# Performance work log

Hardware: AMD Instinct MI355X
Metric: run time of the kernel (lower is better)

Reference implementation:

```python
import jax, jax.numpy as jnp
import numpy as np

N_NODES = 100000
N_EDGES = 1600000
D_IN, D_HID, D_OUT = 64, 128, 64


def setup_inputs() -> dict:
    key = jax.random.key(0)
    ks = jax.random.split(key, 12)
    s = lambda d: 1.0 / np.sqrt(d)
    return {
        "x": jax.random.normal(ks[0], (N_NODES, D_IN), dtype=jnp.float32),
        "edge_index": jax.random.randint(ks[1], (2, N_EDGES), 0, N_NODES, dtype=jnp.int64),
        # conv1 MLP: Linear(D_IN->D_HID), ReLU, Linear(D_HID->D_HID)
        "W1a": jax.random.uniform(ks[2], (D_IN, D_HID), jnp.float32, -s(D_IN), s(D_IN)),
        "b1a": jnp.zeros((D_HID,), jnp.float32),
        "W1b": jax.random.uniform(ks[3], (D_HID, D_HID), jnp.float32, -s(D_HID), s(D_HID)),
        "b1b": jnp.zeros((D_HID,), jnp.float32),
        # conv2 MLP: Linear(D_HID->D_HID), ReLU, Linear(D_HID->D_HID)
        "W2a": jax.random.uniform(ks[4], (D_HID, D_HID), jnp.float32, -s(D_HID), s(D_HID)),
        "b2a": jnp.zeros((D_HID,), jnp.float32),
        "W2b": jax.random.uniform(ks[5], (D_HID, D_HID), jnp.float32, -s(D_HID), s(D_HID)),
        "b2b": jnp.zeros((D_HID,), jnp.float32),
        # final projection Linear(D_HID->D_OUT)
        "Wlin": jax.random.uniform(ks[6], (D_HID, D_OUT), jnp.float32, -s(D_HID), s(D_HID)),
        "blin": jnp.zeros((D_OUT,), jnp.float32),
    }


def _gin_conv(h, src, dst, Wa, ba, Wb, bb, num_nodes):
    # GINConv (eps=0): MLP((1+eps)*x + sum_{j->i} x_j)
    agg = jax.ops.segment_sum(h[src], dst, num_segments=num_nodes)  # [N, d]
    z = h + agg
    z = jax.nn.relu(z @ Wa + ba)
    return z @ Wb + bb


def reference(x, edge_index, W1a, b1a, W1b, b1b, W2a, b2a, W2b, b2b, Wlin, blin):
    n = x.shape[0]
    src, dst = edge_index[0], edge_index[1]
    h = jax.nn.relu(_gin_conv(x, src, dst, W1a, b1a, W1b, b1b, n))
    h = jax.nn.relu(_gin_conv(h, src, dst, W2a, b2a, W2b, b2b, n))
    return h @ Wlin + blin  # [N, D_OUT]
```

## Files before the change

kernel.cpp:

```cpp
#include <hip/hip_runtime.h>
#include <hip/hip_fp16.h>


typedef __attribute__((ext_vector_type(8))) short short8;
typedef __attribute__((ext_vector_type(8))) _Float16 half8;
typedef __attribute__((ext_vector_type(4))) float f32x4;
union F8 { unsigned u[4]; uint4 u4; short8 s; half8 h; };


constexpr int BUCKET_SHIFT = 9;
constexpr int BUCKET_NODES = 1 << BUCKET_SHIFT;
constexpr int CAP = 10240;
constexpr int EPB = 2048;
constexpr int NBUCK_MAX = 256;

__global__ __launch_bounds__(256) void bucket_scatter_kernel(const int* __restrict__ ei, int E,
                                                             int* __restrict__ gcur,
                                                             int* __restrict__ gpk,
                                                             int nbuck) {
    __shared__ int spk[EPB];
    __shared__ unsigned char sbuck[EPB];
    __shared__ int lcnt[NBUCK_MAX];
    __shared__ int lbase[NBUCK_MAX];
    __shared__ int lcur[NBUCK_MAX];
    __shared__ int gbase[NBUCK_MAX];
    __shared__ int stmp[256];

    const int t = threadIdx.x;
    const int e0 = blockIdx.x * EPB;
    const int ecnt = min(EPB, E - e0);

    for (int i = t; i < NBUCK_MAX; i += 256) lcnt[i] = 0;
    __syncthreads();

    for (int i = t; i < ecnt; i += 256) {
        int d = ei[E + e0 + i];
        atomicAdd(&lcnt[d >> BUCKET_SHIFT], 1);
    }
    __syncthreads();

    int v = lcnt[t];
    stmp[t] = v;
    __syncthreads();
    #pragma unroll
    for (int off = 1; off < 256; off <<= 1) {
        int add = (t >= off) ? stmp[t - off] : 0;
        __syncthreads();
        stmp[t] += add;
        __syncthreads();
    }
    lbase[t] = stmp[t] - v;
    lcur[t] = stmp[t] - v;
    __syncthreads();

    for (int i = t; i < ecnt; i += 256) {
        int s = ei[e0 + i];
        int d = ei[E + e0 + i];
        int b = d >> BUCKET_SHIFT;
        int p = atomicAdd(&lcur[b], 1);
        spk[p] = ((d & (BUCKET_NODES - 1)) << 17) | s;
        sbuck[p] = (unsigned char)b;
    }
    __syncthreads();

    if (t < nbuck) {
        int c = lcnt[t];
        gbase[t] = (c > 0) ? atomicAdd(&gcur[t], c) : 0;
    }
    __syncthreads();

    for (int i = t; i < ecnt; i += 256) {
        int b = sbuck[i];
        int gp = gbase[b] + (i - lbase[b]);
        if (gp < (b + 1) * CAP) gpk[gp] = spk[i];
    }
}

__global__ __launch_bounds__(1024) void bucket_build_kernel(const int* __restrict__ gpk,
                                                            const int* __restrict__ gcur,
                                                            int* __restrict__ row_start,
                                                            int* __restrict__ edge_src,
                                                            int N, int E, int nbuck) {
    __shared__ int h[BUCKET_NODES];
    __shared__ int s[BUCKET_NODES];
    __shared__ int sb[NBUCK_MAX];
    __shared__ int bbase_sh;
    const int t = threadIdx.x;
    const int b = blockIdx.x;
    const int base = b << BUCKET_SHIFT;

    if (t < NBUCK_MAX) {
        int c = 0;
        if (t < nbuck) c = min(gcur[t] - t * CAP, CAP);
        sb[t] = c;
    }
    for (int i = t; i < BUCKET_NODES; i += 1024) h[i] = 0;
    __syncthreads();
    #pragma unroll
    for (int off = 1; off < NBUCK_MAX; off <<= 1) {
        int add = (t >= off && t < NBUCK_MAX) ? sb[t - off] : 0;
        __syncthreads();
        if (t < NBUCK_MAX) sb[t] += add;
        __syncthreads();
    }
    if (t == 0) {
        int cb0 = min(gcur[b] - b * CAP, CAP);
        bbase_sh = sb[b] - cb0;
    }

    int cb = min(gcur[b] - b * CAP, CAP);
    const int* pp = gpk + (size_t)b * CAP;
    for (int i = t; i < cb; i += 1024) atomicAdd(&h[((unsigned)pp[i]) >> 17], 1);
    __syncthreads();

    int c0 = (t < BUCKET_NODES) ? h[t] : 0;
    if (t < BUCKET_NODES) s[t] = c0;
    __syncthreads();
    #pragma unroll
    for (int off = 1; off < BUCKET_NODES; off <<= 1) {
        int add = (t >= off && t < BUCKET_NODES) ? s[t - off] : 0;
        __syncthreads();
        if (t < BUCKET_NODES) s[t] += add;
        __syncthreads();
    }
    if (t < BUCKET_NODES) {
        int ex = s[t] - c0 + bbase_sh;
        h[t] = ex;
        if (base + t < N) row_start[base + t] = ex;
    }
    if (b == 0 && t == 0) row_start[N] = E;
    __syncthreads();

    for (int i = t; i < cb; i += 1024) {
        unsigned pw = (unsigned)pp[i];
        int p = atomicAdd(&h[pw >> 17], 1);
        edge_src[p] = (int)(pw & 0x1FFFFu);
    }
}


__global__ __launch_bounds__(256) void prep_kernel(const float* __restrict__ W1a,
                                                   const float* __restrict__ W1b,
                                                   const float* __restrict__ W2a,
                                                   const float* __restrict__ W2b,
                                                   const float* __restrict__ Wlin,
                                                   short* __restrict__ hi,
                                                   const float* __restrict__ x,
                                                   __half2* __restrict__ x16, int n2,
                                                   int* __restrict__ gcur, int nbuck) {
    int i = blockIdx.x * 256 + threadIdx.x;
    if (blockIdx.x == 0 && threadIdx.x < nbuck) gcur[threadIdx.x] = threadIdx.x * CAP;
    if (i < 65536) {
        const float* W;
        int base, K, N;
        if (i < 8192)       { W = W1a;  base = 0;     K = 64;  N = 128; }
        else if (i < 24576) { W = W1b;  base = 8192;  K = 128; N = 128; }
        else if (i < 40960) { W = W2a;  base = 24576; K = 128; N = 128; }
        else if (i < 57344) { W = W2b;  base = 40960; K = 128; N = 128; }
        else                { W = Wlin; base = 57344; K = 128; N = 64;  }
        int rel = i - base;
        int NT = N >> 4;
        int j  = rel & 7;
        int l  = (rel >> 3) & 63;
        int tc = rel >> 9;
        int nt = tc % NT;
        int c  = tc / NT;
        int n  = nt * 16 + (l & 15);
        int k  = c * 32 + ((l >> 4) << 3) + j;
        float v = W[k * N + n];
        hi[i] = (short)__half_as_ushort(__float2half_rn(v));
    }
    for (int k = i; k < n2; k += gridDim.x * 256) {
        float2 v = reinterpret_cast<const float2*>(x)[k];
        x16[k] = __floats2half2_rn(v.x, v.y);
    }
}


__device__ inline void acc8(float* a, const uint4& v) {
    const __half2* h = reinterpret_cast<const __half2*>(&v);
    #pragma unroll
    for (int j = 0; j < 4; ++j) {
        float2 f = __half22float2(h[j]);
        a[2 * j]     += f.x;
        a[2 * j + 1] += f.y;
    }
}

__device__ inline uint4 pack8(const float* a) {
    uint4 o;
    __half2 h;
    h = __floats2half2_rn(a[0], a[1]); o.x = *reinterpret_cast<unsigned*>(&h);
    h = __floats2half2_rn(a[2], a[3]); o.y = *reinterpret_cast<unsigned*>(&h);
    h = __floats2half2_rn(a[4], a[5]); o.z = *reinterpret_cast<unsigned*>(&h);
    h = __floats2half2_rn(a[6], a[7]); o.w = *reinterpret_cast<unsigned*>(&h);
    return o;
}

__global__ __launch_bounds__(256) void agg128_fp16(const __half2* __restrict__ H16,
                                                   const int* __restrict__ row_start,
                                                   const int* __restrict__ edge_src,
                                                   __half2* __restrict__ Z16, int N) {
    int wave = threadIdx.x >> 6, lane = threadIdx.x & 63;
    int node = blockIdx.x * 4 + wave;
    if (node >= N) return;
    const int lg = lane >> 4;
    const int lo = lane & 15;
    const uint4* Hv = reinterpret_cast<const uint4*>(H16);
    int beg = row_start[node], end = row_start[node + 1];

    uint4 selfv = Hv[(size_t)node * 16 + lo];

    float a[8];
    #pragma unroll
    for (int j = 0; j < 8; ++j) a[j] = 0.f;
    if (lg == 0) acc8(a, selfv);

    int i = beg;
    for (; i + 16 <= end; i += 16) {
        int s0 = edge_src[i + lg];
        int s1 = edge_src[i + 4 + lg];
        int s2 = edge_src[i + 8 + lg];
        int s3 = edge_src[i + 12 + lg];
        uint4 v0 = Hv[(size_t)s0 * 16 + lo];
        uint4 v1 = Hv[(size_t)s1 * 16 + lo];
        uint4 v2 = Hv[(size_t)s2 * 16 + lo];
        uint4 v3 = Hv[(size_t)s3 * 16 + lo];
        acc8(a, v0); acc8(a, v1); acc8(a, v2); acc8(a, v3);
    }
    if (i + 8 <= end) {
        int s0 = edge_src[i + lg];
        int s1 = edge_src[i + 4 + lg];
        uint4 v0 = Hv[(size_t)s0 * 16 + lo];
        uint4 v1 = Hv[(size_t)s1 * 16 + lo];
        acc8(a, v0); acc8(a, v1);
        i += 8;
    }
    if (i + 4 <= end) {
        int s0 = edge_src[i + lg];
        uint4 v0 = Hv[(size_t)s0 * 16 + lo];
        acc8(a, v0);
        i += 4;
    }
    int rem = end - i;
    if (lg < rem) {
        int s0 = edge_src[i + lg];
        uint4 v0 = Hv[(size_t)s0 * 16 + lo];
        acc8(a, v0);
    }

    #pragma unroll
    for (int j = 0; j < 8; ++j) {
        a[j] += __shfl_xor(a[j], 16);
        a[j] += __shfl_xor(a[j], 32);
    }

    if (lg == 0) {
        reinterpret_cast<uint4*>(Z16)[(size_t)node * 16 + lo] = pack8(a);
    }
}

__global__ __launch_bounds__(256) void agg64_fp16(const __half2* __restrict__ H16,
                                                  const int* __restrict__ row_start,
                                                  const int* __restrict__ edge_src,
                                                  __half2* __restrict__ Z16, int N) {
    int wave = threadIdx.x >> 6, lane = threadIdx.x & 63;
    int node = blockIdx.x * 4 + wave;
    if (node >= N) return;
    const int lg = lane >> 3;
    const int lo = lane & 7;
    const uint4* Hv = reinterpret_cast<const uint4*>(H16);
    int beg = row_start[node], end = row_start[node + 1];

    uint4 selfv = Hv[(size_t)node * 8 + lo];

    float a[8];
    #pragma unroll
    for (int j = 0; j < 8; ++j) a[j] = 0.f;
    if (lg == 0) acc8(a, selfv);

    int i = beg;
    for (; i + 16 <= end; i += 16) {
        int s0 = edge_src[i + lg];
        int s1 = edge_src[i + 8 + lg];
        uint4 v0 = Hv[(size_t)s0 * 8 + lo];
        uint4 v1 = Hv[(size_t)s1 * 8 + lo];
        acc8(a, v0); acc8(a, v1);
    }
    if (i + 8 <= end) {
        int s0 = edge_src[i + lg];
        uint4 v0 = Hv[(size_t)s0 * 8 + lo];
        acc8(a, v0);
        i += 8;
    }
    int rem = end - i;
    if (lg < rem) {
        int s0 = edge_src[i + lg];
        uint4 v0 = Hv[(size_t)s0 * 8 + lo];
        acc8(a, v0);
    }

    #pragma unroll
    for (int j = 0; j < 8; ++j) {
        a[j] += __shfl_xor(a[j], 8);
        a[j] += __shfl_xor(a[j], 16);
        a[j] += __shfl_xor(a[j], 32);
    }

    if (lg == 0) {
        reinterpret_cast<uint4*>(Z16)[(size_t)node * 8 + lo] = pack8(a);
    }
}


template <int K, int NT>
__device__ inline void compute_directA(const __half2* __restrict__ z, int M, int m0,
                                       const short* __restrict__ WH,
                                       int w, int lane, f32x4 (*acc)[8]) {
    constexpr int KC = K / 32;
    const short8* bhp = reinterpret_cast<const short8*>(WH) + lane;
    const int q = lane >> 4, ln = lane & 15;
    const uint4* zr[2];
    #pragma unroll
    for (int mt = 0; mt < 2; ++mt) {
        int row = m0 + (w * 2 + mt) * 16 + ln;
        if (row >= M) row = M - 1;
        zr[mt] = reinterpret_cast<const uint4*>(z + (size_t)row * (K / 2));
    }
    for (int c = 0; c < KC; ++c) {
        F8 bh[NT];
        #pragma unroll
        for (int nt = 0; nt < NT; ++nt) bh[nt].s = bhp[(c * NT + nt) * 64];
        #pragma unroll
        for (int mt = 0; mt < 2; ++mt) {
            F8 ah;
            ah.u4 = zr[mt][c * 4 + q];
            #pragma unroll
            for (int nt = 0; nt < NT; ++nt) {
                acc[mt][nt] = __builtin_amdgcn_mfma_f32_16x16x32_f16(ah.h, bh[nt].h, acc[mt][nt], 0, 0, 0);
            }
        }
    }
}

template <int K, int NT>
__device__ inline void stage_compute(const unsigned* __restrict__ P,
                                     const short* __restrict__ WH,
                                     int w, int lane, f32x4 (*acc)[8]) {
    constexpr int KC = K / 32;
    const short8* bhp = reinterpret_cast<const short8*>(WH) + lane;
    for (int c = 0; c < KC; ++c) {
        F8 bh[NT];
        #pragma unroll
        for (int nt = 0; nt < NT; ++nt) {
            bh[nt].s = bhp[(c * NT + nt) * 64];
        }
        #pragma unroll
        for (int mt = 0; mt < 2; ++mt) {
            const int T = w * 2 + mt;
            const unsigned* Pb = P + ((T * KC + c) * 8) * 66 + lane;
            unsigned d[8];
            #pragma unroll
            for (int j = 0; j < 8; ++j) d[j] = Pb[j * 66];
            F8 ah;
            #pragma unroll
            for (int j = 0; j < 4; ++j) {
                ah.u[j] = __builtin_amdgcn_perm(d[2 * j + 1], d[2 * j], 0x05040100u);
            }
            #pragma unroll
            for (int nt = 0; nt < NT; ++nt) {
                acc[mt][nt] = __builtin_amdgcn_mfma_f32_16x16x32_f16(ah.h, bh[nt].h, acc[mt][nt], 0, 0, 0);
            }
        }
    }
}

__device__ inline void epilogue_tile(const f32x4* acc, const float* __restrict__ bias,
                                     unsigned* __restrict__ Pout, int T, int lane) {
    int q = lane >> 4, ln = lane & 15;
    #pragma unroll
    for (int nt = 0; nt < 8; ++nt) {
        int col = nt * 16 + ln;
        float b = bias[col];
        int c = col >> 5, jj = col & 7, q2 = (col >> 3) & 3;
        int pb = ((T * 4 + c) * 8 + jj) * 66;
        #pragma unroll
        for (int r = 0; r < 4; ++r) {
            float v = fmaxf(acc[nt][r] + b, 0.f);
            Pout[pb + ((q * 4 + r) | (q2 << 4))] =
                (unsigned)__half_as_ushort(__float2half_rn(v));
        }
    }
}

__global__ __launch_bounds__(256, 2) void mfma_mlp_A(const __half2* __restrict__ z16,
                                                     const short* __restrict__ WaH,
                                                     const float* __restrict__ ba,
                                                     const short* __restrict__ WbH,
                                                     const float* __restrict__ bb,
                                                     __half* __restrict__ H16out, int M) {
    __shared__ unsigned P[8 * 4 * 8 * 66];
    const int t = threadIdx.x;
    const int w = t >> 6, lane = t & 63;
    const int m0 = blockIdx.x * 128;
    const int q = lane >> 4, ln = lane & 15;

    f32x4 acc[2][8];
    #pragma unroll
    for (int mt = 0; mt < 2; ++mt)
        #pragma unroll
        for (int i = 0; i < 8; ++i) acc[mt][i] = (f32x4){0.f, 0.f, 0.f, 0.f};
    compute_directA<64, 8>(z16, M, m0, WaH, w, lane, acc);
    epilogue_tile(acc[0], ba, P, w * 2 + 0, lane);
    epilogue_tile(acc[1], ba, P, w * 2 + 1, lane);

    #pragma unroll
    for (int mt = 0; mt < 2; ++mt)
        #pragma unroll
        for (int i = 0; i < 8; ++i) acc[mt][i] = (f32x4){0.f, 0.f, 0.f, 0.f};
    stage_compute<128, 8>(P, WbH, w, lane, acc);

    #pragma unroll
    for (int mt = 0; mt < 2; ++mt) {
        #pragma unroll
        for (int nt = 0; nt < 8; ++nt) {
            int col = nt * 16 + ln;
            float b = bb[col];
            #pragma unroll
            for (int r = 0; r < 4; ++r) {
                int row = m0 + (w * 2 + mt) * 16 + q * 4 + r;
                if (row < M) {
                    float v = fmaxf(acc[mt][nt][r] + b, 0.f);
                    H16out[(size_t)row * 128 + col] = __float2half_rn(v);
                }
            }
        }
    }
}

__global__ __launch_bounds__(256, 2) void mfma_mlp_B(const __half2* __restrict__ z16,
                                                     const short* __restrict__ WaH,
                                                     const float* __restrict__ ba,
                                                     const short* __restrict__ WbH,
                                                     const float* __restrict__ bb,
                                                     const short* __restrict__ WlH,
                                                     const float* __restrict__ bl,
                                                     float* __restrict__ Out, int M) {
    __shared__ unsigned P[8 * 4 * 8 * 66];
    const int t = threadIdx.x;
    const int w = t >> 6, lane = t & 63;
    const int m0 = blockIdx.x * 128;
    const int q = lane >> 4, ln = lane & 15;

    f32x4 acc[2][8];
    #pragma unroll
    for (int mt = 0; mt < 2; ++mt)
        #pragma unroll
        for (int i = 0; i < 8; ++i) acc[mt][i] = (f32x4){0.f, 0.f, 0.f, 0.f};
    compute_directA<128, 8>(z16, M, m0, WaH, w, lane, acc);
    epilogue_tile(acc[0], ba, P, w * 2 + 0, lane);
    epilogue_tile(acc[1], ba, P, w * 2 + 1, lane);

    #pragma unroll
    for (int mt = 0; mt < 2; ++mt)
        #pragma unroll
        for (int i = 0; i < 8; ++i) acc[mt][i] = (f32x4){0.f, 0.f, 0.f, 0.f};
    stage_compute<128, 8>(P, WbH, w, lane, acc);
    epilogue_tile(acc[0], bb, P, w * 2 + 0, lane);
    epilogue_tile(acc[1], bb, P, w * 2 + 1, lane);

    #pragma unroll
    for (int mt = 0; mt < 2; ++mt)
        #pragma unroll
        for (int i = 0; i < 8; ++i) acc[mt][i] = (f32x4){0.f, 0.f, 0.f, 0.f};
    stage_compute<128, 4>(P, WlH, w, lane, acc);

    #pragma unroll
    for (int mt = 0; mt < 2; ++mt) {
        #pragma unroll
        for (int nt = 0; nt < 4; ++nt) {
            int col = nt * 16 + ln;
            float b = bl[col];
            #pragma unroll
            for (int r = 0; r < 4; ++r) {
                int row = m0 + (w * 2 + mt) * 16 + q * 4 + r;
                if (row < M) Out[(size_t)row * 64 + col] = acc[mt][nt][r] + b;
            }
        }
    }
}


extern "C" void kernel_launch(void* const* d_in, const int* in_sizes, int n_in,
                              void* d_out, int out_size, void* d_ws, size_t ws_size,
                              hipStream_t stream) {
    const float* x    = (const float*)d_in[0];
    const int*   ei   = (const int*)d_in[1];
    const float* W1a  = (const float*)d_in[2];
    const float* b1a  = (const float*)d_in[3];
    const float* W1b  = (const float*)d_in[4];
    const float* b1b  = (const float*)d_in[5];
    const float* W2a  = (const float*)d_in[6];
    const float* b2a  = (const float*)d_in[7];
    const float* W2b  = (const float*)d_in[8];
    const float* b2b  = (const float*)d_in[9];
    const float* Wlin = (const float*)d_in[10];
    const float* blin = (const float*)d_in[11];
    float* out = (float*)d_out;

    const int N = in_sizes[0] / 64;
    const int E = in_sizes[1] / 2;
    const int NBUCK = (N + BUCKET_NODES - 1) >> BUCKET_SHIFT;

    char* ws = (char*)d_ws;
    const size_t bufBytes = (size_t)N * 128 * sizeof(float);
    __half2* Zbuf = (__half2*)(ws + 0);
    char* B = ws + bufBytes;
    size_t off = 3 * bufBytes;
    int* row_start = (int*)(ws + off); off += ((size_t)(N + 1) * 4 + 15) & ~(size_t)15;
    int* cnt       = (int*)(ws + off); off += ((size_t)N * 4 + 15) & ~(size_t)15;
    int* partials  = (int*)(ws + off); off += 4096;
    int* gcur      = (int*)(ws + off); off += 4096;
    int* edge_src  = (int*)(ws + off); off += (size_t)E * 4;
    __half* h116   = (__half*)(ws + off); off += (size_t)N * 128 * 2;
    int* gpk = (int*)B;
    short* wHi = (short*)(B + (32u << 20));
    __half* x16 = (__half*)(B + (36u << 20));
    short* w1aH = wHi + 0;
    short* w1bH = wHi + 8192;
    short* w2aH = wHi + 24576;
    short* w2bH = wHi + 40960;
    short* wlH  = wHi + 57344;
    (void)cnt; (void)partials;

    const int NB_G = (N + 127) / 128;
    const int NB_S = (E + EPB - 1) / EPB;
    const int NB_A128 = (N + 3) / 4;
    const int NB_A64  = (N + 3) / 4;
    const int NB_P = 12500;

    prep_kernel<<<NB_P, 256, 0, stream>>>(W1a, W1b, W2a, W2b, Wlin, wHi,
                                          x, (__half2*)x16, N * 32, gcur, NBUCK);

    bucket_scatter_kernel<<<NB_S, 256, 0, stream>>>(ei, E, gcur, gpk, NBUCK);
    bucket_build_kernel<<<NBUCK, 1024, 0, stream>>>(gpk, gcur, row_start, edge_src,
                                                    N, E, NBUCK);

    agg64_fp16<<<NB_A64, 256, 0, stream>>>((const __half2*)x16, row_start, edge_src, Zbuf, N);
    mfma_mlp_A<<<NB_G, 256, 0, stream>>>(Zbuf, w1aH, b1a, w1bH, b1b, h116, N);

    agg128_fp16<<<NB_A128, 256, 0, stream>>>((const __half2*)h116, row_start, edge_src, Zbuf, N);
    mfma_mlp_B<<<NB_G, 256, 0, stream>>>(Zbuf, w2aH, b2a, w2bH, b2b,
                                         wlH, blin, out, N);
}
```

Before: 311.6 us.

## Fuse prep into scatter kernel and shrink MLP LDS staging to per-wave tiles

The separate prep kernel (weight fp16 packing and x conversion) is merged into the bucket scatter kernel as extra blocks, so the two run concurrently in one launch. The gcur counters are now zeroed by a memset and made bucket-relative. The MLP kernels drop the block-wide shared staging buffer and instead process each 16-row tile through all layers within one wave using a per-wave LDS slice. This halves LDS use and allows 3 blocks per CU instead of 2. It adds a memset launch and relies on the scatter blocks being independent of the prep blocks.

```diff
diff --git a/kernel.cpp b/kernel.cpp
--- a/kernel.cpp
+++ b/kernel.cpp
@@ -14,10 +14,19 @@
 constexpr int EPB = 2048;
 constexpr int NBUCK_MAX = 256;
 
-__global__ __launch_bounds__(256) void bucket_scatter_kernel(const int* __restrict__ ei, int E,
-                                                             int* __restrict__ gcur,
-                                                             int* __restrict__ gpk,
-                                                             int nbuck) {
+__global__ __launch_bounds__(256) void prep_scatter_kernel(const int* __restrict__ ei, int E,
+                                                           int* __restrict__ gcur,
+                                                           int* __restrict__ gpk,
+                                                           int nbuck, int nbs,
+                                                           const float* __restrict__ W1a,
+                                                           const float* __restrict__ W1b,
+                                                           const float* __restrict__ W2a,
+                                                           const float* __restrict__ W2b,
+                                                           const float* __restrict__ Wlin,
+                                                           short* __restrict__ hi,
+                                                           const float* __restrict__ x,
+                                                           __half2* __restrict__ x16, int n2,
+                                                           int npb) {
     __shared__ int spk[EPB];
     __shared__ unsigned char sbuck[EPB];
     __shared__ int lcnt[NBUCK_MAX];
@@ -27,6 +36,37 @@
     __shared__ int stmp[256];
 
     const int t = threadIdx.x;
+
+    if (blockIdx.x >= nbs) {
+        int pb = blockIdx.x - nbs;
+        int i = pb * 256 + t;
+        if (i < 65536) {
+            const float* W;
+            int base, K, N;
+            if (i < 8192)       { W = W1a;  base = 0;     K = 64;  N = 128; }
+            else if (i < 24576) { W = W1b;  base = 8192;  K = 128; N = 128; }
+            else if (i < 40960) { W = W2a;  base = 24576; K = 128; N = 128; }
+            else if (i < 57344) { W = W2b;  base = 40960; K = 128; N = 128; }
+            else                { W = Wlin; base = 57344; K = 128; N = 64;  }
+            int rel = i - base;
+            int NT = N >> 4;
+            int j  = rel & 7;
+            int l  = (rel >> 3) & 63;
+            int tc = rel >> 9;
+            int nt = tc % NT;
+            int c  = tc / NT;
+            int n  = nt * 16 + (l & 15);
+            int k  = c * 32 + ((l >> 4) << 3) + j;
+            float v = W[k * N + n];
+            hi[i] = (short)__half_as_ushort(__float2half_rn(v));
+        }
+        for (int k = i; k < n2; k += npb * 256) {
+            float2 v = reinterpret_cast<const float2*>(x)[k];
+            x16[k] = __floats2half2_rn(v.x, v.y);
+        }
+        return;
+    }
+
     const int e0 = blockIdx.x * EPB;
     const int ecnt = min(EPB, E - e0);
 
@@ -72,7 +112,7 @@
     for (int i = t; i < ecnt; i += 256) {
         int b = sbuck[i];
         int gp = gbase[b] + (i - lbase[b]);
-        if (gp < (b + 1) * CAP) gpk[gp] = spk[i];
+        if (gp < CAP) gpk[(size_t)b * CAP + gp] = spk[i];
     }
 }
 
@@ -91,7 +131,7 @@
 
     if (t < NBUCK_MAX) {
         int c = 0;
-        if (t < nbuck) c = min(gcur[t] - t * CAP, CAP);
+        if (t < nbuck) c = min(gcur[t], CAP);
         sb[t] = c;
     }
     for (int i = t; i < BUCKET_NODES; i += 1024) h[i] = 0;
@@ -104,11 +144,11 @@
         __syncthreads();
     }
     if (t == 0) {
-        int cb0 = min(gcur[b] - b * CAP, CAP);
+        int cb0 = min(gcur[b], CAP);
         bbase_sh = sb[b] - cb0;
     }
 
-    int cb = min(gcur[b] - b * CAP, CAP);
+    int cb = min(gcur[b], CAP);
     const int* pp = gpk + (size_t)b * CAP;
     for (int i = t; i < cb; i += 1024) atomicAdd(&h[((unsigned)pp[i]) >> 17], 1);
     __syncthreads();
@@ -135,44 +175,6 @@
         unsigned pw = (unsigned)pp[i];
         int p = atomicAdd(&h[pw >> 17], 1);
         edge_src[p] = (int)(pw & 0x1FFFFu);
-    }
-}
-
-
-__global__ __launch_bounds__(256) void prep_kernel(const float* __restrict__ W1a,
-                                                   const float* __restrict__ W1b,
-                                                   const float* __restrict__ W2a,
-                                                   const float* __restrict__ W2b,
-                                                   const float* __restrict__ Wlin,
-                                                   short* __restrict__ hi,
-                                                   const float* __restrict__ x,
-                                                   __half2* __restrict__ x16, int n2,
-                                                   int* __restrict__ gcur, int nbuck) {
-    int i = blockIdx.x * 256 + threadIdx.x;
-    if (blockIdx.x == 0 && threadIdx.x < nbuck) gcur[threadIdx.x] = threadIdx.x * CAP;
-    if (i < 65536) {
-        const float* W;
-        int base, K, N;
-        if (i < 8192)       { W = W1a;  base = 0;     K = 64;  N = 128; }
-        else if (i < 24576) { W = W1b;  base = 8192;  K = 128; N = 128; }
-        else if (i < 40960) { W = W2a;  base = 24576; K = 128; N = 128; }
-        else if (i < 57344) { W = W2b;  base = 40960; K = 128; N = 128; }
-        else                { W = Wlin; base = 57344; K = 128; N = 64;  }
-        int rel = i - base;
-        int NT = N >> 4;
-        int j  = rel & 7;
-        int l  = (rel >> 3) & 63;
-        int tc = rel >> 9;
-        int nt = tc % NT;
-        int c  = tc / NT;
-        int n  = nt * 16 + (l & 15);
-        int k  = c * 32 + ((l >> 4) << 3) + j;
-        float v = W[k * N + n];
-        hi[i] = (short)__half_as_ushort(__float2half_rn(v));
-    }
-    for (int k = i; k < n2; k += gridDim.x * 256) {
-        float2 v = reinterpret_cast<const float2*>(x)[k];
-        x16[k] = __floats2half2_rn(v.x, v.y);
     }
 }
 
@@ -343,67 +345,61 @@
     }
 }
 
-template <int K, int NT>
-__device__ inline void stage_compute(const unsigned* __restrict__ P,
-                                     const short* __restrict__ WH,
-                                     int w, int lane, f32x4 (*acc)[8]) {
-    constexpr int KC = K / 32;
-    const short8* bhp = reinterpret_cast<const short8*>(WH) + lane;
-    for (int c = 0; c < KC; ++c) {
-        F8 bh[NT];
-        #pragma unroll
-        for (int nt = 0; nt < NT; ++nt) {
-            bh[nt].s = bhp[(c * NT + nt) * 64];
-        }
-        #pragma unroll
-        for (int mt = 0; mt < 2; ++mt) {
-            const int T = w * 2 + mt;
-            const unsigned* Pb = P + ((T * KC + c) * 8) * 66 + lane;
-            unsigned d[8];
-            #pragma unroll
-            for (int j = 0; j < 8; ++j) d[j] = Pb[j * 66];
-            F8 ah;
-            #pragma unroll
-            for (int j = 0; j < 4; ++j) {
-                ah.u[j] = __builtin_amdgcn_perm(d[2 * j + 1], d[2 * j], 0x05040100u);
-            }
-            #pragma unroll
-            for (int nt = 0; nt < NT; ++nt) {
-                acc[mt][nt] = __builtin_amdgcn_mfma_f32_16x16x32_f16(ah.h, bh[nt].h, acc[mt][nt], 0, 0, 0);
-            }
-        }
-    }
-}
-
-__device__ inline void epilogue_tile(const f32x4* acc, const float* __restrict__ bias,
-                                     unsigned* __restrict__ Pout, int T, int lane) {
+__device__ inline void epilogue_wave(const f32x4* acc, const float* __restrict__ bias,
+                                     unsigned* __restrict__ Pw, int lane) {
     int q = lane >> 4, ln = lane & 15;
     #pragma unroll
     for (int nt = 0; nt < 8; ++nt) {
         int col = nt * 16 + ln;
         float b = bias[col];
         int c = col >> 5, jj = col & 7, q2 = (col >> 3) & 3;
-        int pb = ((T * 4 + c) * 8 + jj) * 66;
+        int pb = (c * 8 + jj) * 66;
         #pragma unroll
         for (int r = 0; r < 4; ++r) {
             float v = fmaxf(acc[nt][r] + b, 0.f);
-            Pout[pb + ((q * 4 + r) | (q2 << 4))] =
+            Pw[pb + ((q * 4 + r) | (q2 << 4))] =
                 (unsigned)__half_as_ushort(__float2half_rn(v));
         }
     }
 }
 
-__global__ __launch_bounds__(256, 2) void mfma_mlp_A(const __half2* __restrict__ z16,
+template <int NT>
+__device__ inline void compute_fromP(const unsigned* __restrict__ Pw,
+                                     const short* __restrict__ WH,
+                                     int lane, f32x4* acc) {
+    const short8* bhp = reinterpret_cast<const short8*>(WH) + lane;
+    for (int c = 0; c < 4; ++c) {
+        F8 bh[NT];
+        #pragma unroll
+        for (int nt = 0; nt < NT; ++nt) bh[nt].s = bhp[(c * NT + nt) * 64];
+        const unsigned* Pb = Pw + (c * 8) * 66 + lane;
+        unsigned d[8];
+        #pragma unroll
+        for (int j = 0; j < 8; ++j) d[j] = Pb[j * 66];
+        F8 ah;
+        #pragma unroll
+        for (int j = 0; j < 4; ++j) {
+            ah.u[j] = __builtin_amdgcn_perm(d[2 * j + 1], d[2 * j], 0x05040100u);
+        }
+        #pragma unroll
+        for (int nt = 0; nt < NT; ++nt) {
+            acc[nt] = __builtin_amdgcn_mfma_f32_16x16x32_f16(ah.h, bh[nt].h, acc[nt], 0, 0, 0);
+        }
+    }
+}
+
+__global__ __launch_bounds__(256, 3) void mfma_mlp_A(const __half2* __restrict__ z16,
                                                      const short* __restrict__ WaH,
                                                      const float* __restrict__ ba,
                                                      const short* __restrict__ WbH,
                                                      const float* __restrict__ bb,
                                                      __half* __restrict__ H16out, int M) {
-    __shared__ unsigned P[8 * 4 * 8 * 66];
+    __shared__ unsigned P[4 * 4 * 8 * 66];
     const int t = threadIdx.x;
     const int w = t >> 6, lane = t & 63;
     const int m0 = blockIdx.x * 128;
     const int q = lane >> 4, ln = lane & 15;
+    unsigned* Pw = P + w * (4 * 8 * 66);
 
     f32x4 acc[2][8];
     #pragma unroll
@@ -411,17 +407,14 @@
         #pragma unroll
         for (int i = 0; i < 8; ++i) acc[mt][i] = (f32x4){0.f, 0.f, 0.f, 0.f};
     compute_directA<64, 8>(z16, M, m0, WaH, w, lane, acc);
-    epilogue_tile(acc[0], ba, P, w * 2 + 0, lane);
-    epilogue_tile(acc[1], ba, P, w * 2 + 1, lane);
-
-    #pragma unroll
-    for (int mt = 0; mt < 2; ++mt)
-        #pragma unroll
-        for (int i = 0; i < 8; ++i) acc[mt][i] = (f32x4){0.f, 0.f, 0.f, 0.f};
-    stage_compute<128, 8>(P, WbH, w, lane, acc);
 
     #pragma unroll
     for (int mt = 0; mt < 2; ++mt) {
+        epilogue_wave(acc[mt], ba, Pw, lane);
+        f32x4 a2[8];
+        #pragma unroll
+        for (int i = 0; i < 8; ++i) a2[i] = (f32x4){0.f, 0.f, 0.f, 0.f};
+        compute_fromP<8>(Pw, WbH, lane, a2);
         #pragma unroll
         for (int nt = 0; nt < 8; ++nt) {
             int col = nt * 16 + ln;
@@ -430,7 +423,7 @@
             for (int r = 0; r < 4; ++r) {
                 int row = m0 + (w * 2 + mt) * 16 + q * 4 + r;
                 if (row < M) {
-                    float v = fmaxf(acc[mt][nt][r] + b, 0.f);
+                    float v = fmaxf(a2[nt][r] + b, 0.f);
                     H16out[(size_t)row * 128 + col] = __float2half_rn(v);
                 }
             }
@@ -438,7 +431,7 @@
     }
 }
 
-__global__ __launch_bounds__(256, 2) void mfma_mlp_B(const __half2* __restrict__ z16,
+__global__ __launch_bounds__(256, 3) void mfma_mlp_B(const __half2* __restrict__ z16,
                                                      const short* __restrict__ WaH,
                                                      const float* __restrict__ ba,
                                                      const short* __restrict__ WbH,
@@ -446,11 +439,12 @@
                                                      const short* __restrict__ WlH,
                                                      const float* __restrict__ bl,
                                                      float* __restrict__ Out, int M) {
-    __shared__ unsigned P[8 * 4 * 8 * 66];
+    __shared__ unsigned P[4 * 4 * 8 * 66];
     const int t = threadIdx.x;
     const int w = t >> 6, lane = t & 63;
     const int m0 = blockIdx.x * 128;
     const int q = lane >> 4, ln = lane & 15;
+    unsigned* Pw = P + w * (4 * 8 * 66);
 
     f32x4 acc[2][8];
     #pragma unroll
@@ -458,25 +452,21 @@
         #pragma unroll
         for (int i = 0; i < 8; ++i) acc[mt][i] = (f32x4){0.f, 0.f, 0.f, 0.f};
     compute_directA<128, 8>(z16, M, m0, WaH, w, lane, acc);
-    epilogue_tile(acc[0], ba, P, w * 2 + 0, lane);
-    epilogue_tile(acc[1], ba, P, w * 2 + 1, lane);
-
-    #pragma unroll
-    for (int mt = 0; mt < 2; ++mt)
-        #pragma unroll
-        for (int i = 0; i < 8; ++i) acc[mt][i] = (f32x4){0.f, 0.f, 0.f, 0.f};
-    stage_compute<128, 8>(P, WbH, w, lane, acc);
-    epilogue_tile(acc[0], bb, P, w * 2 + 0, lane);
-    epilogue_tile(acc[1], bb, P, w * 2 + 1, lane);
-
-    #pragma unroll
-    for (int mt = 0; mt < 2; ++mt)
-        #pragma unroll
-        for (int i = 0; i < 8; ++i) acc[mt][i] = (f32x4){0.f, 0.f, 0.f, 0.f};
-    stage_compute<128, 4>(P, WlH, w, lane, acc);
 
     #pragma unroll
     for (int mt = 0; mt < 2; ++mt) {
+        epilogue_wave(acc[mt], ba, Pw, lane);
+        f32x4 a2[8];
+        #pragma unroll
+        for (int i = 0; i < 8; ++i) a2[i] = (f32x4){0.f, 0.f, 0.f, 0.f};
+        compute_fromP<8>(Pw, WbH, lane, a2);
+
+        epilogue_wave(a2, bb, Pw, lane);
+        f32x4 a3[4];
+        #pragma unroll
+        for (int i = 0; i < 4; ++i) a3[i] = (f32x4){0.f, 0.f, 0.f, 0.f};
+        compute_fromP<4>(Pw, WlH, lane, a3);
+
         #pragma unroll
         for (int nt = 0; nt < 4; ++nt) {
             int col = nt * 16 + ln;
@@ -484,7 +474,7 @@
             #pragma unroll
             for (int r = 0; r < 4; ++r) {
                 int row = m0 + (w * 2 + mt) * 16 + q * 4 + r;
-                if (row < M) Out[(size_t)row * 64 + col] = acc[mt][nt][r] + b;
+                if (row < M) Out[(size_t)row * 64 + col] = a3[nt][r] + b;
             }
         }
     }
@@ -539,10 +529,12 @@
     const int NB_A64  = (N + 3) / 4;
     const int NB_P = 12500;
 
-    prep_kernel<<<NB_P, 256, 0, stream>>>(W1a, W1b, W2a, W2b, Wlin, wHi,
-                                          x, (__half2*)x16, N * 32, gcur, NBUCK);
-
-    bucket_scatter_kernel<<<NB_S, 256, 0, stream>>>(ei, E, gcur, gpk, NBUCK);
+    hipMemsetAsync(gcur, 0, NBUCK_MAX * sizeof(int), stream);
+
+    prep_scatter_kernel<<<NB_S + NB_P, 256, 0, stream>>>(ei, E, gcur, gpk, NBUCK, NB_S,
+                                                         W1a, W1b, W2a, W2b, Wlin, wHi,
+                                                         x, (__half2*)x16, N * 32, NB_P);
+
     bucket_build_kernel<<<NBUCK, 1024, 0, stream>>>(gpk, gcur, row_start, edge_src,
                                                     N, E, NBUCK);
 
```

Measured after the change: 347.5 us. 1.12x slower.
